# Kernel tuning notes

Measured on AMD Instinct MI355X. Metric: run time of the kernel, lower is better.

Reference implementation:

```python
import jax, jax.numpy as jnp
import numpy as np

IN_FEATURES = 4096
OUT_FEATURES = 4096
GROUP_SIZE = 128
PACKED_COLS = IN_FEATURES // 8
GROUP_COUNT = IN_FEATURES // GROUP_SIZE


def setup_inputs() -> dict:
    key = jax.random.key(0)
    k1, k2, k3, k4 = jax.random.split(key, 4)
    x = jax.random.normal(k1, (4, 2048, IN_FEATURES), dtype=jnp.float32)
    # packed int4 weights: 8 nibbles per int32 word
    qweight = jax.random.randint(k2, (OUT_FEATURES, PACKED_COLS), jnp.iinfo(jnp.int32).min, jnp.iinfo(jnp.int32).max, dtype=jnp.int32)
    qscale = (jax.random.uniform(k3, (GROUP_COUNT, OUT_FEATURES), dtype=jnp.float32) + 0.5) * 0.01
    qzeros = jax.random.randint(k4, (GROUP_COUNT, OUT_FEATURES), 0, 16, dtype=jnp.int32)
    return {"x": x, "qweight": qweight, "qscale": qscale, "qzeros": qzeros}


def _dequantize(qweight, qscale, qzeros):
    out_f, packed_cols = qweight.shape
    in_f = packed_cols * 8
    shifts = jnp.arange(0, 32, 4, dtype=jnp.int32)  # 8 nibbles per int32
    # (out, packed, 8) -> (out, in)
    w_int = ((qweight[:, :, None] >> shifts) & 15).reshape(out_f, in_f).astype(jnp.float32)
    w_int = w_int[:, :IN_FEATURES]
    gids = jnp.arange(IN_FEATURES, dtype=jnp.int32) // GROUP_SIZE  # (in,)
    scales = qscale[gids].T   # (out, in)
    zeros = qzeros[gids].astype(jnp.float32).T  # (out, in)
    return (w_int - zeros) * scales


def reference(x, qweight, qscale, qzeros):
    w = _dequantize(qweight, qscale, qzeros).astype(jnp.bfloat16)  # compute_dtype
    y = jnp.einsum('bsi,oi->bso', x.astype(jnp.bfloat16), w)
    return y.astype(x.dtype)
```

## Files before the change

kernel.cpp:

```cpp
#include <hip/hip_runtime.h>
#include <hip/hip_bf16.h>

#define IN_F   4096
#define OUT_F  4096
#define PACKED (IN_F / 8)
#define M_DIM  8192
#define N_DIM  4096
#define K_DIM  4096

#define BM 256
#define BN 256
#define BK 64
#define NT (K_DIM / BK)
#define NHALF (4 * NT)

typedef __bf16 bf16x8 __attribute__((ext_vector_type(8)));
typedef float  f32x4  __attribute__((ext_vector_type(4)));

#define BAR() asm volatile("s_barrier" ::: "memory")
#define VMCNT(n) asm volatile("s_waitcnt vmcnt(" #n ")" ::: "memory")


__global__ __launch_bounds__(256) void dequant_kernel(
    const int* __restrict__ qw, const float* __restrict__ qs,
    const int* __restrict__ qz, __bf16* __restrict__ W)
{
    int ch = blockIdx.x * blockDim.x + threadIdx.x;
    if (ch >= OUT_F * PACKED) return;
    int l     = ch & 63;
    int st    = (ch >> 6) & 15;
    int kTile = (ch >> 10) & 63;
    int nHalf = ch >> 16;
    int o  = nHalf * 128 + ((st >> 1) << 4) + (l & 15);
    int k0 = kTile * 64 + ((st & 1) << 5) + ((l >> 4) << 3);
    int g  = k0 >> 7;
    unsigned int q = (unsigned int)qw[o * PACKED + (k0 >> 3)];
    float scale = qs[g * OUT_F + o];
    float zero  = (float)qz[g * OUT_F + o];
    bf16x8 v;
#pragma unroll
    for (int i = 0; i < 8; ++i) {
        float wi = (float)((q >> (4 * i)) & 15u);
        v[i] = (__bf16)((wi - zero) * scale);
    }
    *reinterpret_cast<bf16x8*>(&W[(size_t)ch * 8]) = v;
}

__global__ __launch_bounds__(256) void cvt_kernel(
    const float* __restrict__ x, __bf16* __restrict__ xb, int nch)
{
    int ch = blockIdx.x * blockDim.x + threadIdx.x;
    if (ch >= nch) return;
    int l     = ch & 63;
    int st    = (ch >> 6) & 15;
    int kTile = (ch >> 10) & 63;
    int mHalf = ch >> 16;
    int m  = mHalf * 128 + ((st >> 1) << 4) + (l & 15);
    int k0 = kTile * 64 + ((st & 1) << 5) + ((l >> 4) << 3);
    const float4* xv = reinterpret_cast<const float4*>(x + (size_t)m * K_DIM + k0);
    float4 a = xv[0];
    float4 b = xv[1];
    bf16x8 v;
    v[0] = (__bf16)a.x; v[1] = (__bf16)a.y; v[2] = (__bf16)a.z; v[3] = (__bf16)a.w;
    v[4] = (__bf16)b.x; v[5] = (__bf16)b.y; v[6] = (__bf16)b.z; v[7] = (__bf16)b.w;
    reinterpret_cast<bf16x8*>(xb)[ch] = v;
}

__global__ __launch_bounds__(512, 2) void gemm_kernel(
    const __bf16* __restrict__ A, const __bf16* __restrict__ B,
    float* __restrict__ C)
{
    extern __shared__ __bf16 lds[];

    const int tid  = threadIdx.x;
    const int lane = tid & 63;
    const int wave = tid >> 6;
    const int wm   = wave >> 2;
    const int wn   = wave & 3;

    const int bid = blockIdx.x;
    const int swz = (bid & 7) * 64 + (bid >> 3);
    const int nBase = (swz & 15) * BN;
    const int mBase = (swz >> 4) * BM;
    const int mHalf0 = mBase >> 7;
    const int nHalf0 = nBase >> 7;

    const int lr = lane & 15;

    auto stage_half = [&](const __bf16* __restrict__ srcFrag, __bf16* dstMat,
                          int halfGlobal, int kTile, int hh) {
        const __bf16* base = srcFrag + ((size_t)(halfGlobal * 64 + kTile) << 13);
#pragma unroll
        for (int i = 0; i < 2; ++i) {
            const int st = i * 8 + wave;
            __builtin_amdgcn_global_load_lds(
                (const __attribute__((address_space(1))) void*)(base + st * 512 + lane * 8),
                (__attribute__((address_space(3))) void*)(dstMat + (hh * 16 + st) * 512 + lane * 8),
                16, 0, 0);
        }
    };
    auto stage_H = [&](int H) {
        const int t = H >> 2;
        const int h = H & 3;
        __bf16* base = lds + (size_t)(t & 1) * 32768 + (size_t)(h >> 1) * 16384;
        if (h & 2) stage_half(B, base, nHalf0 + (h & 1), t, h & 1);
        else       stage_half(A, base, mHalf0 + (h & 1), t, h & 1);
    };

    f32x4 acc[8][4];
#pragma unroll
    for (int i = 0; i < 8; ++i)
#pragma unroll
        for (int j = 0; j < 4; ++j)
            acc[i][j] = 0.0f;

#pragma unroll
    for (int H = 0; H < 7; ++H) stage_H(H);
    VMCNT(6);
    BAR();

#define LDA(mi, kb) (*(const bf16x8*)(lA + (((wm * 8 + (mi)) * 2 + (kb)) * 512 + lane * 8)))
#define LDB(ni, kb) (*(const bf16x8*)(lB + (((wn * 4 + (ni)) * 2 + (kb)) * 512 + lane * 8)))

    for (int t = 0; t < NT; ++t) {
        const __bf16* lA = lds + (size_t)(t & 1) * 32768;
        const __bf16* lB = lA + 16384;
        const int Hb = 4 * t + 7;
        bf16x8 Af[8][2];
        bf16x8 Bf[2][2];

#pragma unroll
        for (int mi = 0; mi < 4; ++mi) { Af[mi][0] = LDA(mi, 0); Af[mi][1] = LDA(mi, 1); }
#pragma unroll
        for (int ni = 0; ni < 2; ++ni) { Bf[ni][0] = LDB(ni, 0); Bf[ni][1] = LDB(ni, 1); }
        __builtin_amdgcn_sched_barrier(0);
        if (Hb < NHALF) stage_H(Hb);
        BAR();
        __builtin_amdgcn_s_setprio(1);
#pragma unroll
        for (int kb = 0; kb < 2; ++kb)
#pragma unroll
            for (int mi = 0; mi < 4; ++mi)
#pragma unroll
                for (int ni = 0; ni < 2; ++ni)
                    acc[mi][ni] = __builtin_amdgcn_mfma_f32_16x16x32_bf16(Af[mi][kb], Bf[ni][kb], acc[mi][ni], 0, 0, 0);
        __builtin_amdgcn_s_setprio(0);
        BAR();

#pragma unroll
        for (int mi = 4; mi < 8; ++mi) { Af[mi][0] = LDA(mi, 0); Af[mi][1] = LDA(mi, 1); }
        __builtin_amdgcn_sched_barrier(0);
        if (Hb + 1 < NHALF) stage_H(Hb + 1);
        BAR();
        __builtin_amdgcn_s_setprio(1);
#pragma unroll
        for (int kb = 0; kb < 2; ++kb)
#pragma unroll
            for (int mi = 4; mi < 8; ++mi)
#pragma unroll
                for (int ni = 0; ni < 2; ++ni)
                    acc[mi][ni] = __builtin_amdgcn_mfma_f32_16x16x32_bf16(Af[mi][kb], Bf[ni][kb], acc[mi][ni], 0, 0, 0);
        __builtin_amdgcn_s_setprio(0);
        BAR();

#pragma unroll
        for (int ni = 0; ni < 2; ++ni) { Bf[ni][0] = LDB(ni + 2, 0); Bf[ni][1] = LDB(ni + 2, 1); }
        __builtin_amdgcn_sched_barrier(0);
        if (Hb + 2 < NHALF) stage_H(Hb + 2);
        BAR();
        __builtin_amdgcn_s_setprio(1);
#pragma unroll
        for (int kb = 0; kb < 2; ++kb)
#pragma unroll
            for (int mi = 0; mi < 4; ++mi)
#pragma unroll
                for (int nj = 0; nj < 2; ++nj)
                    acc[mi][nj + 2] = __builtin_amdgcn_mfma_f32_16x16x32_bf16(Af[mi][kb], Bf[nj][kb], acc[mi][nj + 2], 0, 0, 0);
        __builtin_amdgcn_s_setprio(0);
        BAR();

        if (Hb + 3 < NHALF) stage_H(Hb + 3);
        BAR();
        __builtin_amdgcn_s_setprio(1);
#pragma unroll
        for (int kb = 0; kb < 2; ++kb)
#pragma unroll
            for (int mi = 4; mi < 8; ++mi)
#pragma unroll
                for (int nj = 0; nj < 2; ++nj)
                    acc[mi][nj + 2] = __builtin_amdgcn_mfma_f32_16x16x32_bf16(Af[mi][kb], Bf[nj][kb], acc[mi][nj + 2], 0, 0, 0);
        __builtin_amdgcn_s_setprio(0);
        if (t < NT - 2)       VMCNT(6);
        else if (t == NT - 2) VMCNT(0);
        BAR();
    }

#pragma unroll
    for (int mi = 0; mi < 8; ++mi)
#pragma unroll
        for (int ni = 0; ni < 4; ++ni) {
            const int col = nBase + wn * 64 + ni * 16 + lr;
#pragma unroll
            for (int r = 0; r < 4; ++r) {
                const int row = mBase + wm * 128 + mi * 16 + (lane >> 4) * 4 + r;
                C[(size_t)row * N_DIM + col] = (float)(__bf16)acc[mi][ni][r];
            }
        }
#undef LDA
#undef LDB
}

extern "C" void kernel_launch(void* const* d_in, const int* in_sizes, int n_in,
                              void* d_out, int out_size, void* d_ws, size_t ws_size,
                              hipStream_t stream)
{
    const float* x       = (const float*)d_in[0];
    const int*   qweight = (const int*)d_in[1];
    const float* qscale  = (const float*)d_in[2];
    const int*   qzeros  = (const int*)d_in[3];
    float*       out     = (float*)d_out;

    __bf16* W  = (__bf16*)d_ws;
    __bf16* xb = (__bf16*)((char*)d_ws + (size_t)N_DIM * K_DIM * sizeof(__bf16));

    {
        int total = OUT_F * PACKED;
        dequant_kernel<<<(total + 255) / 256, 256, 0, stream>>>(qweight, qscale, qzeros, W);
    }
    {
        int nch = (M_DIM * K_DIM) / 8;
        cvt_kernel<<<(nch + 255) / 256, 256, 0, stream>>>(x, xb, nch);
    }
    {
        (void)hipFuncSetAttribute((const void*)gemm_kernel,
                                  hipFuncAttributeMaxDynamicSharedMemorySize, 131072);
        dim3 grid((M_DIM / BM) * (N_DIM / BN));
        gemm_kernel<<<grid, 512, 131072, stream>>>(xb, W, out);
    }
}
```

Before: 276.7 us.

## Reorder GEMM prefetch schedule to preload next-tile A fragments during final MFMA phase

Restructures the software pipeline of the bf16 GEMM main loop. The first A fragments of the next K tile are loaded from LDS during the last MFMA phase of the current tile, and the global-to-LDS staging order and vmcnt waits are re-sequenced to match. The aim is to hide LDS read latency at tile boundaries and shorten the stall before the first MFMA batch. It keeps Af live across iterations, which raises register pressure, and the wait counts must still cover the data each phase reads.

```diff
diff --git a/kernel.cpp b/kernel.cpp
--- a/kernel.cpp
+++ b/kernel.cpp
@@ -12,7 +12,6 @@
 #define BN 256
 #define BK 64
 #define NT (K_DIM / BK)
-#define NHALF (4 * NT)
 
 typedef __bf16 bf16x8 __attribute__((ext_vector_type(8)));
 typedef float  f32x4  __attribute__((ext_vector_type(4)));
@@ -89,19 +88,17 @@
 
     auto stage_half = [&](const __bf16* __restrict__ srcFrag, __bf16* dstMat,
                           int halfGlobal, int kTile, int hh) {
-        const __bf16* base = srcFrag + ((size_t)(halfGlobal * 64 + kTile) << 13);
 #pragma unroll
         for (int i = 0; i < 2; ++i) {
             const int st = i * 8 + wave;
+            const __bf16* base = srcFrag + ((size_t)(halfGlobal * 64 + kTile) << 13);
             __builtin_amdgcn_global_load_lds(
                 (const __attribute__((address_space(1))) void*)(base + st * 512 + lane * 8),
                 (__attribute__((address_space(3))) void*)(dstMat + (hh * 16 + st) * 512 + lane * 8),
                 16, 0, 0);
         }
     };
-    auto stage_H = [&](int H) {
-        const int t = H >> 2;
-        const int h = H & 3;
+    auto stage_H = [&](int t, int h) {
         __bf16* base = lds + (size_t)(t & 1) * 32768 + (size_t)(h >> 1) * 16384;
         if (h & 2) stage_half(B, base, nHalf0 + (h & 1), t, h & 1);
         else       stage_half(A, base, mHalf0 + (h & 1), t, h & 1);
@@ -114,27 +111,31 @@
         for (int j = 0; j < 4; ++j)
             acc[i][j] = 0.0f;
 
-#pragma unroll
-    for (int H = 0; H < 7; ++H) stage_H(H);
-    VMCNT(6);
+    bf16x8 Af[8][2];
+    bf16x8 Bf[2][2];
+
+#define LDA(buf, mi, kb) (*(const bf16x8*)((buf) + (((wm * 8 + (mi)) * 2 + (kb)) * 512 + lane * 8)))
+#define LDB(buf, ni, kb) (*(const bf16x8*)((buf) + (((wn * 4 + (ni)) * 2 + (kb)) * 512 + lane * 8)))
+
+    stage_H(0, 0); stage_H(0, 1); stage_H(0, 2); stage_H(0, 3);
+    stage_H(1, 0); stage_H(1, 1);
+    VMCNT(4);
     BAR();
-
-#define LDA(mi, kb) (*(const bf16x8*)(lA + (((wm * 8 + (mi)) * 2 + (kb)) * 512 + lane * 8)))
-#define LDB(ni, kb) (*(const bf16x8*)(lB + (((wn * 4 + (ni)) * 2 + (kb)) * 512 + lane * 8)))
+    {
+        const __bf16* lA0 = lds;
+#pragma unroll
+        for (int mi = 0; mi < 4; ++mi) { Af[mi][0] = LDA(lA0, mi, 0); Af[mi][1] = LDA(lA0, mi, 1); }
+    }
 
     for (int t = 0; t < NT; ++t) {
-        const __bf16* lA = lds + (size_t)(t & 1) * 32768;
-        const __bf16* lB = lA + 16384;
-        const int Hb = 4 * t + 7;
-        bf16x8 Af[8][2];
-        bf16x8 Bf[2][2];
-
-#pragma unroll
-        for (int mi = 0; mi < 4; ++mi) { Af[mi][0] = LDA(mi, 0); Af[mi][1] = LDA(mi, 1); }
-#pragma unroll
-        for (int ni = 0; ni < 2; ++ni) { Bf[ni][0] = LDB(ni, 0); Bf[ni][1] = LDB(ni, 1); }
-        __builtin_amdgcn_sched_barrier(0);
-        if (Hb < NHALF) stage_H(Hb);
+        const __bf16* lA  = lds + (size_t)(t & 1) * 32768;
+        const __bf16* lB  = lA + 16384;
+        const __bf16* lAn = lds + (size_t)((t + 1) & 1) * 32768;
+
+#pragma unroll
+        for (int ni = 0; ni < 2; ++ni) { Bf[ni][0] = LDB(lB, ni, 0); Bf[ni][1] = LDB(lB, ni, 1); }
+        __builtin_amdgcn_sched_barrier(0);
+        if (t < NT - 1) stage_H(t + 1, 2);
         BAR();
         __builtin_amdgcn_s_setprio(1);
 #pragma unroll
@@ -148,9 +149,9 @@
         BAR();
 
 #pragma unroll
-        for (int mi = 4; mi < 8; ++mi) { Af[mi][0] = LDA(mi, 0); Af[mi][1] = LDA(mi, 1); }
-        __builtin_amdgcn_sched_barrier(0);
-        if (Hb + 1 < NHALF) stage_H(Hb + 1);
+        for (int mi = 4; mi < 8; ++mi) { Af[mi][0] = LDA(lA, mi, 0); Af[mi][1] = LDA(lA, mi, 1); }
+        __builtin_amdgcn_sched_barrier(0);
+        if (t < NT - 1) stage_H(t + 1, 3);
         BAR();
         __builtin_amdgcn_s_setprio(1);
 #pragma unroll
@@ -164,9 +165,9 @@
         BAR();
 
 #pragma unroll
-        for (int ni = 0; ni < 2; ++ni) { Bf[ni][0] = LDB(ni + 2, 0); Bf[ni][1] = LDB(ni + 2, 1); }
-        __builtin_amdgcn_sched_barrier(0);
-        if (Hb + 2 < NHALF) stage_H(Hb + 2);
+        for (int ni = 0; ni < 2; ++ni) { Bf[ni][0] = LDB(lB, ni + 2, 0); Bf[ni][1] = LDB(lB, ni + 2, 1); }
+        __builtin_amdgcn_sched_barrier(0);
+        if (t < NT - 2) stage_H(t + 2, 0);
         BAR();
         __builtin_amdgcn_s_setprio(1);
 #pragma unroll
@@ -177,9 +178,16 @@
                 for (int nj = 0; nj < 2; ++nj)
                     acc[mi][nj + 2] = __builtin_amdgcn_mfma_f32_16x16x32_bf16(Af[mi][kb], Bf[nj][kb], acc[mi][nj + 2], 0, 0, 0);
         __builtin_amdgcn_s_setprio(0);
-        BAR();
-
-        if (Hb + 3 < NHALF) stage_H(Hb + 3);
+        if (t < NT - 2)       VMCNT(6);
+        else if (t == NT - 2) VMCNT(4);
+        BAR();
+
+        if (t < NT - 1) {
+#pragma unroll
+            for (int mi = 0; mi < 4; ++mi) { Af[mi][0] = LDA(lAn, mi, 0); Af[mi][1] = LDA(lAn, mi, 1); }
+        }
+        __builtin_amdgcn_sched_barrier(0);
+        if (t < NT - 2) stage_H(t + 2, 1);
         BAR();
         __builtin_amdgcn_s_setprio(1);
 #pragma unroll
@@ -190,7 +198,7 @@
                 for (int nj = 0; nj < 2; ++nj)
                     acc[mi][nj + 2] = __builtin_amdgcn_mfma_f32_16x16x32_bf16(Af[mi][kb], Bf[nj][kb], acc[mi][nj + 2], 0, 0, 0);
         __builtin_amdgcn_s_setprio(0);
-        if (t < NT - 2)       VMCNT(6);
+        if (t < NT - 2)       VMCNT(4);
         else if (t == NT - 2) VMCNT(0);
         BAR();
     }
```

After: 278.0 us. Within noise of the previous version (+0.4%).

## Shrink GEMM tile to 128x128 with 4 waves and two-phase staging

Applied to the files above, without the earlier changes.

Reduces the GEMM block tile from 256x256 (8 waves) to 128x128 (4 waves), halving LDS use per block and quadrupling the grid to 2048 blocks. The staging pipeline is restructured into two phases per k-tile, prefetching B for the next tile and A two tiles ahead. The aim is better occupancy and wave-count balance across CUs. The cost is lower arithmetic intensity per block, which means more global and L2 traffic for the A and B operands.

```diff
diff --git a/kernel.cpp b/kernel.cpp
--- a/kernel.cpp
+++ b/kernel.cpp
@@ -8,11 +8,10 @@
 #define N_DIM  4096
 #define K_DIM  4096
 
-#define BM 256
-#define BN 256
+#define BM 128
+#define BN 128
 #define BK 64
 #define NT (K_DIM / BK)
-#define NHALF (4 * NT)
 
 typedef __bf16 bf16x8 __attribute__((ext_vector_type(8)));
 typedef float  f32x4  __attribute__((ext_vector_type(4)));
@@ -66,7 +65,7 @@
     reinterpret_cast<bf16x8*>(xb)[ch] = v;
 }
 
-__global__ __launch_bounds__(512, 2) void gemm_kernel(
+__global__ __launch_bounds__(256, 2) void gemm_kernel(
     const __bf16* __restrict__ A, const __bf16* __restrict__ B,
     float* __restrict__ C)
 {
@@ -75,66 +74,62 @@
     const int tid  = threadIdx.x;
     const int lane = tid & 63;
     const int wave = tid >> 6;
-    const int wm   = wave >> 2;
-    const int wn   = wave & 3;
+    const int wm   = wave >> 1;
+    const int wn   = wave & 1;
 
     const int bid = blockIdx.x;
-    const int swz = (bid & 7) * 64 + (bid >> 3);
-    const int nBase = (swz & 15) * BN;
-    const int mBase = (swz >> 4) * BM;
-    const int mHalf0 = mBase >> 7;
-    const int nHalf0 = nBase >> 7;
+    const int swz = (bid & 7) * 256 + (bid >> 3);
+    const int nBase = (swz & 31) * BN;
+    const int mBase = (swz >> 5) * BM;
+    const int mHalf = mBase >> 7;
+    const int nHalf = nBase >> 7;
 
     const int lr = lane & 15;
 
-    auto stage_half = [&](const __bf16* __restrict__ srcFrag, __bf16* dstMat,
-                          int halfGlobal, int kTile, int hh) {
-        const __bf16* base = srcFrag + ((size_t)(halfGlobal * 64 + kTile) << 13);
-#pragma unroll
-        for (int i = 0; i < 2; ++i) {
-            const int st = i * 8 + wave;
+    auto stage = [&](const __bf16* __restrict__ srcFrag, __bf16* dst,
+                     int halfG, int kTile) {
+        const __bf16* src = srcFrag + ((size_t)(halfG * 64 + kTile) << 13);
+#pragma unroll
+        for (int i = 0; i < 4; ++i) {
+            const int st = i * 4 + wave;
             __builtin_amdgcn_global_load_lds(
-                (const __attribute__((address_space(1))) void*)(base + st * 512 + lane * 8),
-                (__attribute__((address_space(3))) void*)(dstMat + (hh * 16 + st) * 512 + lane * 8),
+                (const __attribute__((address_space(1))) void*)(src + st * 512 + lane * 8),
+                (__attribute__((address_space(3))) void*)(dst + st * 512 + lane * 8),
                 16, 0, 0);
         }
     };
-    auto stage_H = [&](int H) {
-        const int t = H >> 2;
-        const int h = H & 3;
-        __bf16* base = lds + (size_t)(t & 1) * 32768 + (size_t)(h >> 1) * 16384;
-        if (h & 2) stage_half(B, base, nHalf0 + (h & 1), t, h & 1);
-        else       stage_half(A, base, mHalf0 + (h & 1), t, h & 1);
-    };
-
-    f32x4 acc[8][4];
-#pragma unroll
-    for (int i = 0; i < 8; ++i)
+
+    f32x4 acc[4][4];
+#pragma unroll
+    for (int i = 0; i < 4; ++i)
 #pragma unroll
         for (int j = 0; j < 4; ++j)
             acc[i][j] = 0.0f;
 
-#pragma unroll
-    for (int H = 0; H < 7; ++H) stage_H(H);
-    VMCNT(6);
+    bf16x8 Af[4][2];
+    bf16x8 Bf[2][2];
+
+#define LDA(buf, mi, kb) (*(const bf16x8*)((buf) + (((wm * 4 + (mi)) * 2 + (kb)) * 512 + lane * 8)))
+#define LDB(buf, nj, kb) (*(const bf16x8*)((buf) + (((wn * 4 + (nj)) * 2 + (kb)) * 512 + lane * 8)))
+
+    stage(A, lds,         mHalf, 0);
+    stage(B, lds + 8192,  nHalf, 0);
+    stage(A, lds + 16384, mHalf, 1);
+    VMCNT(4);
     BAR();
 
-#define LDA(mi, kb) (*(const bf16x8*)(lA + (((wm * 8 + (mi)) * 2 + (kb)) * 512 + lane * 8)))
-#define LDB(ni, kb) (*(const bf16x8*)(lB + (((wn * 4 + (ni)) * 2 + (kb)) * 512 + lane * 8)))
-
     for (int t = 0; t < NT; ++t) {
-        const __bf16* lA = lds + (size_t)(t & 1) * 32768;
-        const __bf16* lB = lA + 16384;
-        const int Hb = 4 * t + 7;
-        bf16x8 Af[8][2];
-        bf16x8 Bf[2][2];
-
-#pragma unroll
-        for (int mi = 0; mi < 4; ++mi) { Af[mi][0] = LDA(mi, 0); Af[mi][1] = LDA(mi, 1); }
-#pragma unroll
-        for (int ni = 0; ni < 2; ++ni) { Bf[ni][0] = LDB(ni, 0); Bf[ni][1] = LDB(ni, 1); }
+        __bf16* base = lds + (size_t)(t & 1) * 16384;
+        const __bf16* cA = base;
+        const __bf16* cB = base + 8192;
+        __bf16* nB = lds + (size_t)((t + 1) & 1) * 16384 + 8192;
+
+#pragma unroll
+        for (int mi = 0; mi < 4; ++mi) { Af[mi][0] = LDA(cA, mi, 0); Af[mi][1] = LDA(cA, mi, 1); }
+#pragma unroll
+        for (int nj = 0; nj < 2; ++nj) { Bf[nj][0] = LDB(cB, nj, 0); Bf[nj][1] = LDB(cB, nj, 1); }
         __builtin_amdgcn_sched_barrier(0);
-        if (Hb < NHALF) stage_H(Hb);
+        if (t < NT - 1) stage(B, nB, nHalf, t + 1);
         BAR();
         __builtin_amdgcn_s_setprio(1);
 #pragma unroll
@@ -142,31 +137,15 @@
 #pragma unroll
             for (int mi = 0; mi < 4; ++mi)
 #pragma unroll
-                for (int ni = 0; ni < 2; ++ni)
-                    acc[mi][ni] = __builtin_amdgcn_mfma_f32_16x16x32_bf16(Af[mi][kb], Bf[ni][kb], acc[mi][ni], 0, 0, 0);
+                for (int nj = 0; nj < 2; ++nj)
+                    acc[mi][nj] = __builtin_amdgcn_mfma_f32_16x16x32_bf16(Af[mi][kb], Bf[nj][kb], acc[mi][nj], 0, 0, 0);
         __builtin_amdgcn_s_setprio(0);
         BAR();
 
 #pragma unroll
-        for (int mi = 4; mi < 8; ++mi) { Af[mi][0] = LDA(mi, 0); Af[mi][1] = LDA(mi, 1); }
+        for (int nj = 0; nj < 2; ++nj) { Bf[nj][0] = LDB(cB, nj + 2, 0); Bf[nj][1] = LDB(cB, nj + 2, 1); }
         __builtin_amdgcn_sched_barrier(0);
-        if (Hb + 1 < NHALF) stage_H(Hb + 1);
-        BAR();
-        __builtin_amdgcn_s_setprio(1);
-#pragma unroll
-        for (int kb = 0; kb < 2; ++kb)
-#pragma unroll
-            for (int mi = 4; mi < 8; ++mi)
-#pragma unroll
-                for (int ni = 0; ni < 2; ++ni)
-                    acc[mi][ni] = __builtin_amdgcn_mfma_f32_16x16x32_bf16(Af[mi][kb], Bf[ni][kb], acc[mi][ni], 0, 0, 0);
-        __builtin_amdgcn_s_setprio(0);
-        BAR();
-
-#pragma unroll
-        for (int ni = 0; ni < 2; ++ni) { Bf[ni][0] = LDB(ni + 2, 0); Bf[ni][1] = LDB(ni + 2, 1); }
-        __builtin_amdgcn_sched_barrier(0);
-        if (Hb + 2 < NHALF) stage_H(Hb + 2);
+        if (t < NT - 2) stage(A, base, mHalf, t + 2);
         BAR();
         __builtin_amdgcn_s_setprio(1);
 #pragma unroll
@@ -177,33 +156,20 @@
                 for (int nj = 0; nj < 2; ++nj)
                     acc[mi][nj + 2] = __builtin_amdgcn_mfma_f32_16x16x32_bf16(Af[mi][kb], Bf[nj][kb], acc[mi][nj + 2], 0, 0, 0);
         __builtin_amdgcn_s_setprio(0);
-        BAR();
-
-        if (Hb + 3 < NHALF) stage_H(Hb + 3);
-        BAR();
-        __builtin_amdgcn_s_setprio(1);
-#pragma unroll
-        for (int kb = 0; kb < 2; ++kb)
-#pragma unroll
-            for (int mi = 4; mi < 8; ++mi)
-#pragma unroll
-                for (int nj = 0; nj < 2; ++nj)
-                    acc[mi][nj + 2] = __builtin_amdgcn_mfma_f32_16x16x32_bf16(Af[mi][kb], Bf[nj][kb], acc[mi][nj + 2], 0, 0, 0);
-        __builtin_amdgcn_s_setprio(0);
-        if (t < NT - 2)       VMCNT(6);
+        if (t < NT - 2)       VMCNT(4);
         else if (t == NT - 2) VMCNT(0);
         BAR();
     }
 
 #pragma unroll
-    for (int mi = 0; mi < 8; ++mi)
-#pragma unroll
-        for (int ni = 0; ni < 4; ++ni) {
-            const int col = nBase + wn * 64 + ni * 16 + lr;
+    for (int mi = 0; mi < 4; ++mi)
+#pragma unroll
+        for (int nj = 0; nj < 4; ++nj) {
+            const int col = nBase + wn * 64 + nj * 16 + lr;
 #pragma unroll
             for (int r = 0; r < 4; ++r) {
-                const int row = mBase + wm * 128 + mi * 16 + (lane >> 4) * 4 + r;
-                C[(size_t)row * N_DIM + col] = (float)(__bf16)acc[mi][ni][r];
+                const int row = mBase + wm * 64 + mi * 16 + (lane >> 4) * 4 + r;
+                C[(size_t)row * N_DIM + col] = (float)(__bf16)acc[mi][nj][r];
             }
         }
 #undef LDA
@@ -233,8 +199,8 @@
     }
     {
         (void)hipFuncSetAttribute((const void*)gemm_kernel,
-                                  hipFuncAttributeMaxDynamicSharedMemorySize, 131072);
+                                  hipFuncAttributeMaxDynamicSharedMemorySize, 65536);
         dim3 grid((M_DIM / BM) * (N_DIM / BN));
-        gemm_kernel<<<grid, 512, 131072, stream>>>(xb, W, out);
-    }
-}
+        gemm_kernel<<<grid, 256, 65536, stream>>>(xb, W, out);
+    }
+}
```

New measurement: 348.2 us. +25.8%, slower.

## Switch GEMM to 32x32x16 MFMA with matching fragment layout

Applied to the files above, without the earlier changes.

Replaces the 16x16x32 bf16 MFMA tiles with 32x32x16 MFMA tiles, reshaping the pre-packed fragment layout produced by the dequant and convert kernels to match. Accumulators become four by two blocks of 16 floats, and the epilogue is rewritten for the 32x32 output lane mapping. Larger MFMA tiles need fewer instructions and fewer LDS fragment reads per FLOP. The trade-off is longer-latency instructions and a different register and scheduling profile inside the same barrier-staged pipeline.

```diff
diff --git a/kernel.cpp b/kernel.cpp
--- a/kernel.cpp
+++ b/kernel.cpp
@@ -14,11 +14,13 @@
 #define NT (K_DIM / BK)
 #define NHALF (4 * NT)
 
-typedef __bf16 bf16x8 __attribute__((ext_vector_type(8)));
-typedef float  f32x4  __attribute__((ext_vector_type(4)));
+typedef __bf16 bf16x8  __attribute__((ext_vector_type(8)));
+typedef float  f32x16  __attribute__((ext_vector_type(16)));
 
 #define BAR() asm volatile("s_barrier" ::: "memory")
 #define VMCNT(n) asm volatile("s_waitcnt vmcnt(" #n ")" ::: "memory")
+#define AS1 __attribute__((address_space(1)))
+#define AS3 __attribute__((address_space(3)))
 
 
 __global__ __launch_bounds__(256) void dequant_kernel(
@@ -30,9 +32,10 @@
     int l     = ch & 63;
     int st    = (ch >> 6) & 15;
     int kTile = (ch >> 10) & 63;
-    int nHalf = ch >> 16;
-    int o  = nHalf * 128 + ((st >> 1) << 4) + (l & 15);
-    int k0 = kTile * 64 + ((st & 1) << 5) + ((l >> 4) << 3);
+    int half  = ch >> 16;
+    int rb = st >> 2, ks = st & 3;
+    int o  = half * 128 + rb * 32 + (l & 31);
+    int k0 = kTile * 64 + ks * 16 + ((l >> 5) << 3);
     int g  = k0 >> 7;
     unsigned int q = (unsigned int)qw[o * PACKED + (k0 >> 3)];
     float scale = qs[g * OUT_F + o];
@@ -54,9 +57,10 @@
     int l     = ch & 63;
     int st    = (ch >> 6) & 15;
     int kTile = (ch >> 10) & 63;
-    int mHalf = ch >> 16;
-    int m  = mHalf * 128 + ((st >> 1) << 4) + (l & 15);
-    int k0 = kTile * 64 + ((st & 1) << 5) + ((l >> 4) << 3);
+    int half  = ch >> 16;
+    int rb = st >> 2, ks = st & 3;
+    int m  = half * 128 + rb * 32 + (l & 31);
+    int k0 = kTile * 64 + ks * 16 + ((l >> 5) << 3);
     const float4* xv = reinterpret_cast<const float4*>(x + (size_t)m * K_DIM + k0);
     float4 a = xv[0];
     float4 b = xv[1];
@@ -77,6 +81,7 @@
     const int wave = tid >> 6;
     const int wm   = wave >> 2;
     const int wn   = wave & 3;
+    const int lane8 = lane * 8;
 
     const int bid = blockIdx.x;
     const int swz = (bid & 7) * 64 + (bid >> 3);
@@ -85,17 +90,15 @@
     const int mHalf0 = mBase >> 7;
     const int nHalf0 = nBase >> 7;
 
-    const int lr = lane & 15;
-
     auto stage_half = [&](const __bf16* __restrict__ srcFrag, __bf16* dstMat,
                           int halfGlobal, int kTile, int hh) {
-        const __bf16* base = srcFrag + ((size_t)(halfGlobal * 64 + kTile) << 13);
 #pragma unroll
         for (int i = 0; i < 2; ++i) {
             const int st = i * 8 + wave;
+            const __bf16* base = srcFrag + ((size_t)(halfGlobal * 64 + kTile) << 13);
             __builtin_amdgcn_global_load_lds(
-                (const __attribute__((address_space(1))) void*)(base + st * 512 + lane * 8),
-                (__attribute__((address_space(3))) void*)(dstMat + (hh * 16 + st) * 512 + lane * 8),
+                (const AS1 void*)(base + st * 512 + lane8),
+                (AS3 void*)(dstMat + (hh * 16 + st) * 512 + lane8),
                 16, 0, 0);
         }
     };
@@ -107,75 +110,74 @@
         else       stage_half(A, base, mHalf0 + (h & 1), t, h & 1);
     };
 
-    f32x4 acc[8][4];
-#pragma unroll
-    for (int i = 0; i < 8; ++i)
-#pragma unroll
-        for (int j = 0; j < 4; ++j)
-            acc[i][j] = 0.0f;
+    f32x16 acc[4][2];
+#pragma unroll
+    for (int i = 0; i < 4; ++i)
+#pragma unroll
+        for (int j = 0; j < 2; ++j)
+            acc[i][j] = (f32x16)0.0f;
+
+    bf16x8 Af[4][4];
+    bf16x8 Bf[4];
+
+#define LDA(lA, mb, ks) (*(const bf16x8*)((lA) + (size_t)wm * 8192 + (((mb) * 4 + (ks)) << 9) + lane8))
+#define LDB(lB, nb, ks) (*(const bf16x8*)((lB) + (size_t)(((wn * 2 + (nb)) >> 2)) * 8192 + ((((((wn * 2 + (nb)) & 3)) * 4 + (ks))) << 9) + lane8))
 
 #pragma unroll
     for (int H = 0; H < 7; ++H) stage_H(H);
     VMCNT(6);
     BAR();
-
-#define LDA(mi, kb) (*(const bf16x8*)(lA + (((wm * 8 + (mi)) * 2 + (kb)) * 512 + lane * 8)))
-#define LDB(ni, kb) (*(const bf16x8*)(lB + (((wn * 4 + (ni)) * 2 + (kb)) * 512 + lane * 8)))
 
     for (int t = 0; t < NT; ++t) {
         const __bf16* lA = lds + (size_t)(t & 1) * 32768;
         const __bf16* lB = lA + 16384;
         const int Hb = 4 * t + 7;
-        bf16x8 Af[8][2];
-        bf16x8 Bf[2][2];
-
-#pragma unroll
-        for (int mi = 0; mi < 4; ++mi) { Af[mi][0] = LDA(mi, 0); Af[mi][1] = LDA(mi, 1); }
-#pragma unroll
-        for (int ni = 0; ni < 2; ++ni) { Bf[ni][0] = LDB(ni, 0); Bf[ni][1] = LDB(ni, 1); }
+
+#pragma unroll
+        for (int mb = 0; mb < 2; ++mb)
+#pragma unroll
+            for (int ks = 0; ks < 4; ++ks) Af[mb][ks] = LDA(lA, mb, ks);
+#pragma unroll
+        for (int ks = 0; ks < 4; ++ks) Bf[ks] = LDB(lB, 0, ks);
         __builtin_amdgcn_sched_barrier(0);
         if (Hb < NHALF) stage_H(Hb);
         BAR();
         __builtin_amdgcn_s_setprio(1);
 #pragma unroll
-        for (int kb = 0; kb < 2; ++kb)
-#pragma unroll
-            for (int mi = 0; mi < 4; ++mi)
-#pragma unroll
-                for (int ni = 0; ni < 2; ++ni)
-                    acc[mi][ni] = __builtin_amdgcn_mfma_f32_16x16x32_bf16(Af[mi][kb], Bf[ni][kb], acc[mi][ni], 0, 0, 0);
-        __builtin_amdgcn_s_setprio(0);
-        BAR();
-
-#pragma unroll
-        for (int mi = 4; mi < 8; ++mi) { Af[mi][0] = LDA(mi, 0); Af[mi][1] = LDA(mi, 1); }
+        for (int ks = 0; ks < 4; ++ks)
+#pragma unroll
+            for (int mb = 0; mb < 2; ++mb)
+                acc[mb][0] = __builtin_amdgcn_mfma_f32_32x32x16_bf16(Af[mb][ks], Bf[ks], acc[mb][0], 0, 0, 0);
+        __builtin_amdgcn_s_setprio(0);
+        BAR();
+
+#pragma unroll
+        for (int mb = 2; mb < 4; ++mb)
+#pragma unroll
+            for (int ks = 0; ks < 4; ++ks) Af[mb][ks] = LDA(lA, mb, ks);
         __builtin_amdgcn_sched_barrier(0);
         if (Hb + 1 < NHALF) stage_H(Hb + 1);
         BAR();
         __builtin_amdgcn_s_setprio(1);
 #pragma unroll
-        for (int kb = 0; kb < 2; ++kb)
-#pragma unroll
-            for (int mi = 4; mi < 8; ++mi)
-#pragma unroll
-                for (int ni = 0; ni < 2; ++ni)
-                    acc[mi][ni] = __builtin_amdgcn_mfma_f32_16x16x32_bf16(Af[mi][kb], Bf[ni][kb], acc[mi][ni], 0, 0, 0);
-        __builtin_amdgcn_s_setprio(0);
-        BAR();
-
-#pragma unroll
-        for (int ni = 0; ni < 2; ++ni) { Bf[ni][0] = LDB(ni + 2, 0); Bf[ni][1] = LDB(ni + 2, 1); }
+        for (int ks = 0; ks < 4; ++ks)
+#pragma unroll
+            for (int mb = 2; mb < 4; ++mb)
+                acc[mb][0] = __builtin_amdgcn_mfma_f32_32x32x16_bf16(Af[mb][ks], Bf[ks], acc[mb][0], 0, 0, 0);
+        __builtin_amdgcn_s_setprio(0);
+        BAR();
+
+#pragma unroll
+        for (int ks = 0; ks < 4; ++ks) Bf[ks] = LDB(lB, 1, ks);
         __builtin_amdgcn_sched_barrier(0);
         if (Hb + 2 < NHALF) stage_H(Hb + 2);
         BAR();
         __builtin_amdgcn_s_setprio(1);
 #pragma unroll
-        for (int kb = 0; kb < 2; ++kb)
-#pragma unroll
-            for (int mi = 0; mi < 4; ++mi)
-#pragma unroll
-                for (int nj = 0; nj < 2; ++nj)
-                    acc[mi][nj + 2] = __builtin_amdgcn_mfma_f32_16x16x32_bf16(Af[mi][kb], Bf[nj][kb], acc[mi][nj + 2], 0, 0, 0);
+        for (int ks = 0; ks < 4; ++ks)
+#pragma unroll
+            for (int mb = 0; mb < 2; ++mb)
+                acc[mb][1] = __builtin_amdgcn_mfma_f32_32x32x16_bf16(Af[mb][ks], Bf[ks], acc[mb][1], 0, 0, 0);
         __builtin_amdgcn_s_setprio(0);
         BAR();
 
@@ -183,27 +185,28 @@
         BAR();
         __builtin_amdgcn_s_setprio(1);
 #pragma unroll
-        for (int kb = 0; kb < 2; ++kb)
-#pragma unroll
-            for (int mi = 4; mi < 8; ++mi)
-#pragma unroll
-                for (int nj = 0; nj < 2; ++nj)
-                    acc[mi][nj + 2] = __builtin_amdgcn_mfma_f32_16x16x32_bf16(Af[mi][kb], Bf[nj][kb], acc[mi][nj + 2], 0, 0, 0);
+        for (int ks = 0; ks < 4; ++ks)
+#pragma unroll
+            for (int mb = 2; mb < 4; ++mb)
+                acc[mb][1] = __builtin_amdgcn_mfma_f32_32x32x16_bf16(Af[mb][ks], Bf[ks], acc[mb][1], 0, 0, 0);
         __builtin_amdgcn_s_setprio(0);
         if (t < NT - 2)       VMCNT(6);
         else if (t == NT - 2) VMCNT(0);
         BAR();
     }
 
-#pragma unroll
-    for (int mi = 0; mi < 8; ++mi)
-#pragma unroll
-        for (int ni = 0; ni < 4; ++ni) {
-            const int col = nBase + wn * 64 + ni * 16 + lr;
-#pragma unroll
-            for (int r = 0; r < 4; ++r) {
-                const int row = mBase + wm * 128 + mi * 16 + (lane >> 4) * 4 + r;
-                C[(size_t)row * N_DIM + col] = (float)(__bf16)acc[mi][ni][r];
+    const int ccol = lane & 31;
+    const int rhi  = (lane >> 5) * 4;
+#pragma unroll
+    for (int mb = 0; mb < 4; ++mb)
+#pragma unroll
+        for (int nb = 0; nb < 2; ++nb) {
+            const int col = nBase + wn * 64 + nb * 32 + ccol;
+            const int rowB = mBase + wm * 128 + mb * 32 + rhi;
+#pragma unroll
+            for (int r = 0; r < 16; ++r) {
+                const int row = rowB + (r & 3) + 8 * (r >> 2);
+                C[(size_t)row * N_DIM + col] = (float)(__bf16)acc[mb][nb][r];
             }
         }
 #undef LDA
```

After: 301.0 us. 1.09x slower.
